# Kernel optimization log

Hardware: AMD Instinct MI355X
Metric: run time of the kernel (lower is better)

## Reference

```python
import jax, jax.numpy as jnp
import numpy as np

H = 16   # num_heads
A = 64   # attn_size
D = 1024 # dims
NEG = -1000000000.0


def setup_inputs() -> dict:
    key = jax.random.key(0)
    k1, k2, k3, k4 = jax.random.split(key, 4)
    B, S = 2, 2048
    qs = jax.random.normal(k1, (B, S, D), dtype=jnp.float32)
    mask = jax.random.randint(k2, (B, S), 0, 2, dtype=jnp.int32)
    Wqkv = jax.random.normal(k3, (D, 3 * H * A), dtype=jnp.float32) * (1.0 / np.sqrt(D))
    Wout = jax.random.normal(k4, (H * A, D), dtype=jnp.float32) * (1.0 / np.sqrt(H * A))
    bout = jnp.zeros((D,), dtype=jnp.float32)
    return {"qs": qs, "mask": mask, "Wqkv": Wqkv, "Wout": Wout, "bout": bout}


def reference(qs, mask, Wqkv, Wout, bout):
    B, S, _ = qs.shape
    qkv = qs @ Wqkv                              # [B,S,3*H*A]
    qkv = qkv.reshape(B, S, 3 * H, A)            # split axis=2 in thirds (TF layout)
    q = jnp.transpose(qkv[:, :, 0:H, :], (0, 2, 1, 3))        # [B,H,S,A]
    k = jnp.transpose(qkv[:, :, H:2 * H, :], (0, 2, 1, 3))    # [B,H,S,A]
    v = jnp.transpose(qkv[:, :, 2 * H:3 * H, :], (0, 2, 1, 3))# [B,H,S,A]
    scores = jnp.einsum('bhqa,bhka->bhqk', q, k) / jnp.sqrt(jnp.float32(A))
    m = mask[:, None, None, :]                   # [B,1,1,S] broadcast over heads, queries
    scores = jnp.where(m == 0, NEG, scores)
    probs = jax.nn.softmax(scores, axis=-1)      # dropout_prob=0 / inference -> identity
    ctx = jnp.einsum('bhqk,bhka->bhqa', probs, v)  # [B,H,S,A]
    ctx = jnp.transpose(ctx, (0, 2, 1, 3)).reshape(B, S, H * A)
    return ctx @ Wout + bout
```

## Files before the change

kernel.cpp:

```cpp
#include <hip/hip_runtime.h>
#include <stdint.h>


typedef unsigned short u16;
typedef uint32_t u32;
typedef u16   u16x4  __attribute__((ext_vector_type(4)));
typedef u16   u16x8  __attribute__((ext_vector_type(8)));
typedef __bf16 bf16x8 __attribute__((ext_vector_type(8)));
typedef float f32x4  __attribute__((ext_vector_type(4)));

#define DEV __device__ __forceinline__

DEV u16 cvt_bf(float f) {
    return __builtin_bit_cast(u16, (__bf16)f);
}

DEV void async16(const void* g, void* l) {
    __builtin_amdgcn_global_load_lds(
        reinterpret_cast<const uint32_t __attribute__((address_space(1)))*>(
            reinterpret_cast<uintptr_t>(g)),
        reinterpret_cast<uint32_t __attribute__((address_space(3)))*>(
            reinterpret_cast<uintptr_t>(l)),
        16, 0, 0);
}

DEV f32x4 mfma16(bf16x8 a, bf16x8 b, f32x4 c) {
    return __builtin_amdgcn_mfma_f32_16x16x32_bf16(a, b, c, 0, 0, 0);
}


__global__ void k_prep(const float* __restrict__ qs, u16* __restrict__ qs_bf,
                       const int* __restrict__ m, float* __restrict__ bias,
                       const float* __restrict__ Wqkv, u16* __restrict__ WqkvT,
                       const float* __restrict__ Wout, u16* __restrict__ WoutT) {
    __shared__ float t[32][33];
    int bid = blockIdx.x;
    if (bid < 4096) {
        int i = (bid * 256 + threadIdx.x) * 4;
        float4 v = *reinterpret_cast<const float4*>(qs + i);
        u16x4 o = { cvt_bf(v.x), cvt_bf(v.y), cvt_bf(v.z), cvt_bf(v.w) };
        *reinterpret_cast<u16x4*>(qs_bf + i) = o;
        return;
    }
    if (bid < 4112) {
        int i = (bid - 4096) * 256 + threadIdx.x;
        bias[i] = m[i] ? 0.0f : -1.0e9f;
        return;
    }
    const float* src; u16* dst; int R, C, bx, by;
    if (bid < 7184) { int q = bid - 4112; src = Wqkv; dst = WqkvT; R = 1024; C = 3072; bx = q % 96; by = q / 96; }
    else            { int q = bid - 7184; src = Wout; dst = WoutT; R = 1024; C = 1024; bx = q % 32; by = q / 32; }
    int c0 = bx * 32, r0 = by * 32;
    int tx = threadIdx.x & 31, ty = threadIdx.x >> 5;
#pragma unroll
    for (int i = 0; i < 4; ++i)
        t[ty + 8 * i][tx] = src[(size_t)(r0 + ty + 8 * i) * C + c0 + tx];
    __syncthreads();
#pragma unroll
    for (int i = 0; i < 4; ++i)
        dst[(size_t)(c0 + ty + 8 * i) * R + r0 + tx] = cvt_bf(t[tx][ty + 8 * i]);
}


template <int BM, int BN, bool OUT_BF16, bool HAS_BIAS>
__global__ __launch_bounds__(256, 3) void k_gemm(
    const u16* __restrict__ A, const u16* __restrict__ Bt,
    void* __restrict__ Cv, const float* __restrict__ bias,
    int M, int N, int K)
{
    constexpr int MT = BM / 32, NT = BN / 32;
    __shared__ __attribute__((aligned(16))) u16 As[2][BM * 32];
    __shared__ __attribute__((aligned(16))) u16 Bs[2][BN * 32];

    const int tid = threadIdx.x, wave = tid >> 6, lane = tid & 63;
    const int lh = lane & 15, lg = lane >> 4;
    const int nbn = N / BN;

    const int nwg = gridDim.x;
    const int q8 = nwg >> 3, r8 = nwg & 7;
    const int xcd = blockIdx.x & 7, li = blockIdx.x >> 3;
    const int wg = (xcd < r8 ? xcd * (q8 + 1) : r8 * (q8 + 1) + (xcd - r8) * q8) + li;

    const int m0 = (wg / nbn) * BM, n0 = (wg % nbn) * BN;
    const int wm = wave >> 1, wn = wave & 1;
    const int nk = K >> 5;

    auto stage = [&](int buf, int kt) {
#pragma unroll
        for (int i = 0; i < BM / 64; ++i) {
            int c = i * 256 + tid;
            int row = c >> 2, cc = c & 3;
            int sc = cc ^ (row & 3);
            async16(A + (size_t)(m0 + row) * K + kt * 32 + sc * 8, &As[buf][c * 8]);
        }
#pragma unroll
        for (int i = 0; i < BN / 64; ++i) {
            int c = i * 256 + tid;
            int row = c >> 2, cc = c & 3;
            int sc = cc ^ (row & 3);
            async16(Bt + (size_t)(n0 + row) * K + kt * 32 + sc * 8, &Bs[buf][c * 8]);
        }
    };

    f32x4 acc[MT][NT] = {};
    stage(0, 0);
    __syncthreads();
    int buf = 0;
    for (int kt = 0; kt < nk; ++kt) {
        if (kt + 1 < nk) stage(buf ^ 1, kt + 1);
        bf16x8 af[MT], bf_[NT];
#pragma unroll
        for (int mt = 0; mt < MT; ++mt) {
            int row = wm * (BM / 2) + mt * 16 + lh;
            int off = row * 32 + ((lg ^ (row & 3)) * 8);
            af[mt] = __builtin_bit_cast(bf16x8,
                     *reinterpret_cast<const u16x8*>(&As[buf][off]));
        }
#pragma unroll
        for (int nt = 0; nt < NT; ++nt) {
            int row = wn * (BN / 2) + nt * 16 + lh;
            int off = row * 32 + ((lg ^ (row & 3)) * 8);
            bf_[nt] = __builtin_bit_cast(bf16x8,
                      *reinterpret_cast<const u16x8*>(&Bs[buf][off]));
        }
        __builtin_amdgcn_s_setprio(1);
#pragma unroll
        for (int mt = 0; mt < MT; ++mt)
#pragma unroll
            for (int nt = 0; nt < NT; ++nt)
                acc[mt][nt] = mfma16(af[mt], bf_[nt], acc[mt][nt]);
        __builtin_amdgcn_s_setprio(0);
        __syncthreads();
        buf ^= 1;
    }

#pragma unroll
    for (int mt = 0; mt < MT; ++mt)
#pragma unroll
        for (int nt = 0; nt < NT; ++nt) {
            int col = n0 + wn * (BN / 2) + nt * 16 + lh;
#pragma unroll
            for (int r = 0; r < 4; ++r) {
                int row = m0 + wm * (BM / 2) + mt * 16 + 4 * lg + r;
                float v = acc[mt][nt][r];
                if (HAS_BIAS) v += bias[col];
                if (OUT_BF16) ((u16*)Cv)[(size_t)row * N + col] = cvt_bf(v);
                else          ((float*)Cv)[(size_t)row * N + col] = v;
            }
        }
}


__global__ __launch_bounds__(512, 4) void k_attn(
    const u16* __restrict__ qkv, const float* __restrict__ biasg, u16* __restrict__ ctx)
{
    __shared__ __attribute__((aligned(16))) u16 Ks[2][64 * 64];
    __shared__ __attribute__((aligned(16))) u16 Vt[2][64 * 72];
    __shared__ __attribute__((aligned(16))) u16 Ps[8 * 16 * 72];

    const int tid = threadIdx.x, wave = tid >> 6, lane = tid & 63;
    const int lh = lane & 15, lg = lane >> 4;

    const int wg = (blockIdx.x & 7) * 64 + (blockIdx.x >> 3);
    const int qt = wg & 15, bh = wg >> 4;
    const int b = bh >> 4, h = bh & 15;

    const u16* qbase = qkv + ((size_t)b * 2048 * 48 + h) * 64;
    const u16* kbase = qkv + ((size_t)b * 2048 * 48 + 16 + h) * 64;
    const u16* vbase = qkv + ((size_t)b * 2048 * 48 + 32 + h) * 64;
    const float* brow = biasg + b * 2048;

    const int srow = wave * 8 + (lane >> 3);
    const int scc  = lane & 7;
    const int ksrc = scc ^ (srow & 7);
    const int vswz = srow ^ (scc << 3);

    bf16x8 qf[2];
    {
        int row = qt * 128 + wave * 16 + lh;
        qf[0] = __builtin_bit_cast(bf16x8,
            *reinterpret_cast<const u16x8*>(qbase + (size_t)row * 3072 + lg * 8));
        qf[1] = __builtin_bit_cast(bf16x8,
            *reinterpret_cast<const u16x8*>(qbase + (size_t)row * 3072 + 32 + lg * 8));
    }

    f32x4 oa[4] = {};
    float lst[4] = {0.0f, 0.0f, 0.0f, 0.0f};

    u16* Pw = &Ps[wave * 16 * 72];

    {
        async16(kbase + (size_t)srow * 3072 + ksrc * 8, &Ks[0][wave * 512]);
        u16x8 v = *reinterpret_cast<const u16x8*>(vbase + (size_t)srow * 3072 + scc * 8);
#pragma unroll
        for (int j = 0; j < 8; ++j) Vt[0][(scc * 8 + j) * 72 + vswz] = v[j];
    }

    for (int kt = 0; kt < 32; ++kt) {
        __syncthreads();
        const int buf = kt & 1;
        if (kt + 1 < 32) {
            async16(kbase + (size_t)((kt + 1) * 64 + srow) * 3072 + ksrc * 8, &Ks[buf ^ 1][wave * 512]);
            u16x8 v = *reinterpret_cast<const u16x8*>(
                vbase + (size_t)((kt + 1) * 64 + srow) * 3072 + scc * 8);
#pragma unroll
            for (int j = 0; j < 8; ++j) Vt[buf ^ 1][(scc * 8 + j) * 72 + vswz] = v[j];
        }

        float biasv[4];
#pragma unroll
        for (int nt = 0; nt < 4; ++nt) biasv[nt] = brow[kt * 64 + nt * 16 + lh];

        f32x4 sa[4] = {};
        __builtin_amdgcn_s_setprio(1);
#pragma unroll
        for (int ks = 0; ks < 2; ++ks) {
            bf16x8 kb[4];
#pragma unroll
            for (int nt = 0; nt < 4; ++nt) {
                int row = nt * 16 + lh;
                int off = row * 64 + (((ks * 4 + lg) ^ (row & 7)) << 3);
                kb[nt] = __builtin_bit_cast(bf16x8,
                         *reinterpret_cast<const u16x8*>(&Ks[buf][off]));
            }
#pragma unroll
            for (int nt = 0; nt < 4; ++nt)
                sa[nt] = mfma16(qf[ks], kb[nt], sa[nt]);
        }
        __builtin_amdgcn_s_setprio(0);

#pragma unroll
        for (int nt = 0; nt < 4; ++nt)
#pragma unroll
            for (int r = 0; r < 4; ++r) {
                float e = __expf(fmaf(sa[nt][r], 0.125f, biasv[nt]));
                lst[r] += e;
                Pw[(4 * lg + r) * 72 + nt * 16 + lh] = cvt_bf(e);
            }

        __builtin_amdgcn_s_setprio(1);
#pragma unroll
        for (int ks = 0; ks < 2; ++ks) {
            bf16x8 pa = __builtin_bit_cast(bf16x8,
                        *reinterpret_cast<const u16x8*>(Pw + lh * 72 + ks * 32 + lg * 8));
            bf16x8 vb[4];
#pragma unroll
            for (int nt = 0; nt < 4; ++nt) {
                int col = nt * 16 + lh;
                int g = (col >> 3) & 7;
                int off = col * 72 + (((ks * 4 + lg) ^ g) << 3);
                vb[nt] = __builtin_bit_cast(bf16x8,
                         *reinterpret_cast<const u16x8*>(&Vt[buf][off]));
            }
#pragma unroll
            for (int nt = 0; nt < 4; ++nt)
                oa[nt] = mfma16(pa, vb[nt], oa[nt]);
        }
        __builtin_amdgcn_s_setprio(0);
    }

#pragma unroll
    for (int r = 0; r < 4; ++r) {
        float s = lst[r];
#pragma unroll
        for (int o = 1; o < 16; o <<= 1) s += __shfl_xor(s, o);
        lst[r] = 1.0f / s;
    }

#pragma unroll
    for (int nt = 0; nt < 4; ++nt)
#pragma unroll
        for (int r = 0; r < 4; ++r) {
            int row = qt * 128 + wave * 16 + 4 * lg + r;
            ctx[(size_t)(b * 2048 + row) * 1024 + h * 64 + nt * 16 + lh] = cvt_bf(oa[nt][r] * lst[r]);
        }
}


extern "C" void kernel_launch(void* const* d_in, const int* in_sizes, int n_in,
                              void* d_out, int out_size, void* d_ws, size_t ws_size,
                              hipStream_t stream)
{
    const float* qs   = (const float*)d_in[0];
    const int*   mask = (const int*)d_in[1];
    const float* Wqkv = (const float*)d_in[2];
    const float* Wout = (const float*)d_in[3];
    const float* bout = (const float*)d_in[4];
    float* out = (float*)d_out;

    char* ws = (char*)d_ws;
    u16*   qs_bf = (u16*)(ws);
    u16*   WqkvT = (u16*)(ws + 8388608);
    u16*   WoutT = (u16*)(ws + 14680064);
    u16*   qkvb  = (u16*)(ws + 16777216);
    u16*   ctxb  = (u16*)(ws + 41943040);
    float* biasb = (float*)(ws + 50331648);

    k_prep<<<8208, 256, 0, stream>>>(qs, qs_bf, mask, biasb, Wqkv, WqkvT, Wout, WoutT);

    k_gemm<128, 128, true, false><<<768, 256, 0, stream>>>(qs_bf, WqkvT, qkvb, nullptr, 4096, 3072, 1024);
    k_attn<<<512, 512, 0, stream>>>(qkvb, biasb, ctxb);
    k_gemm<128, 64, false, true><<<512, 256, 0, stream>>>(ctxb, WoutT, out, bout, 4096, 1024, 1024);
}
```

Baseline: 193.5 us.

## Give each attention wave two query tiles and halve the workgroup size

The attention kernel now runs 4 waves per workgroup instead of 8, and each wave handles 32 query rows (two 16-row MFMA tiles). The K and V fragments read from LDS are then reused across both query tiles, which halves LDS reads per MFMA. The K/V tile loads are split across the fewer threads. In exchange each wave holds more accumulator registers, and the launch bound drops to 3 workgroups per CU, so there are fewer waves available to hide latency.

Measured after the change: 194.8 us. Within noise of the previous version (+0.7%).

```diff
diff --git a/kernel.cpp b/kernel.cpp
--- a/kernel.cpp
+++ b/kernel.cpp
@@ -151,12 +151,12 @@
 }
 
 
-__global__ __launch_bounds__(512, 4) void k_attn(
+__global__ __launch_bounds__(256, 3) void k_attn(
     const u16* __restrict__ qkv, const float* __restrict__ biasg, u16* __restrict__ ctx)
 {
     __shared__ __attribute__((aligned(16))) u16 Ks[2][64 * 64];
     __shared__ __attribute__((aligned(16))) u16 Vt[2][64 * 72];
-    __shared__ __attribute__((aligned(16))) u16 Ps[8 * 16 * 72];
+    __shared__ __attribute__((aligned(16))) u16 Ps[4 * 32 * 72];
 
     const int tid = threadIdx.x, wave = tid >> 6, lane = tid & 63;
     const int lh = lane & 15, lg = lane >> 4;
@@ -170,48 +170,59 @@
     const u16* vbase = qkv + ((size_t)b * 2048 * 48 + 32 + h) * 64;
     const float* brow = biasg + b * 2048;
 
-    const int srow = wave * 8 + (lane >> 3);
-    const int scc  = lane & 7;
-    const int ksrc = scc ^ (srow & 7);
-    const int vswz = srow ^ (scc << 3);
-
-    bf16x8 qf[2];
-    {
-        int row = qt * 128 + wave * 16 + lh;
-        qf[0] = __builtin_bit_cast(bf16x8,
+    int srow_[2], scc_[2];
+#pragma unroll
+    for (int i = 0; i < 2; ++i) {
+        int c = (wave * 2 + i) * 64 + lane;
+        srow_[i] = c >> 3; scc_[i] = c & 7;
+    }
+
+    bf16x8 qf[2][2];
+#pragma unroll
+    for (int mt = 0; mt < 2; ++mt) {
+        int row = qt * 128 + wave * 32 + mt * 16 + lh;
+        qf[mt][0] = __builtin_bit_cast(bf16x8,
             *reinterpret_cast<const u16x8*>(qbase + (size_t)row * 3072 + lg * 8));
-        qf[1] = __builtin_bit_cast(bf16x8,
+        qf[mt][1] = __builtin_bit_cast(bf16x8,
             *reinterpret_cast<const u16x8*>(qbase + (size_t)row * 3072 + 32 + lg * 8));
     }
 
-    f32x4 oa[4] = {};
-    float lst[4] = {0.0f, 0.0f, 0.0f, 0.0f};
-
-    u16* Pw = &Ps[wave * 16 * 72];
-
-    {
-        async16(kbase + (size_t)srow * 3072 + ksrc * 8, &Ks[0][wave * 512]);
+    f32x4 oa[2][4] = {};
+    float lst[2][4] = {};
+
+    u16* Pw = &Ps[wave * 32 * 72];
+
+#pragma unroll
+    for (int i = 0; i < 2; ++i) {
+        int srow = srow_[i], scc = scc_[i];
+        async16(kbase + (size_t)srow * 3072 + (scc ^ (srow & 7)) * 8, &Ks[0][(wave * 2 + i) * 512]);
         u16x8 v = *reinterpret_cast<const u16x8*>(vbase + (size_t)srow * 3072 + scc * 8);
 #pragma unroll
-        for (int j = 0; j < 8; ++j) Vt[0][(scc * 8 + j) * 72 + vswz] = v[j];
+        for (int j = 0; j < 8; ++j) Vt[0][(scc * 8 + j) * 72 + (srow ^ (scc << 3))] = v[j];
     }
 
     for (int kt = 0; kt < 32; ++kt) {
         __syncthreads();
         const int buf = kt & 1;
         if (kt + 1 < 32) {
-            async16(kbase + (size_t)((kt + 1) * 64 + srow) * 3072 + ksrc * 8, &Ks[buf ^ 1][wave * 512]);
-            u16x8 v = *reinterpret_cast<const u16x8*>(
-                vbase + (size_t)((kt + 1) * 64 + srow) * 3072 + scc * 8);
-#pragma unroll
-            for (int j = 0; j < 8; ++j) Vt[buf ^ 1][(scc * 8 + j) * 72 + vswz] = v[j];
+#pragma unroll
+            for (int i = 0; i < 2; ++i) {
+                int srow = srow_[i], scc = scc_[i];
+                async16(kbase + (size_t)((kt + 1) * 64 + srow) * 3072 + (scc ^ (srow & 7)) * 8,
+                        &Ks[buf ^ 1][(wave * 2 + i) * 512]);
+                u16x8 v = *reinterpret_cast<const u16x8*>(
+                    vbase + (size_t)((kt + 1) * 64 + srow) * 3072 + scc * 8);
+#pragma unroll
+                for (int j = 0; j < 8; ++j)
+                    Vt[buf ^ 1][(scc * 8 + j) * 72 + (srow ^ (scc << 3))] = v[j];
+            }
         }
 
         float biasv[4];
 #pragma unroll
         for (int nt = 0; nt < 4; ++nt) biasv[nt] = brow[kt * 64 + nt * 16 + lh];
 
-        f32x4 sa[4] = {};
+        f32x4 sa[2][4] = {};
         __builtin_amdgcn_s_setprio(1);
 #pragma unroll
         for (int ks = 0; ks < 2; ++ks) {
@@ -224,56 +235,68 @@
                          *reinterpret_cast<const u16x8*>(&Ks[buf][off]));
             }
 #pragma unroll
+            for (int mt = 0; mt < 2; ++mt)
+#pragma unroll
+                for (int nt = 0; nt < 4; ++nt)
+                    sa[mt][nt] = mfma16(qf[mt][ks], kb[nt], sa[mt][nt]);
+        }
+        __builtin_amdgcn_s_setprio(0);
+
+#pragma unroll
+        for (int mt = 0; mt < 2; ++mt)
+#pragma unroll
             for (int nt = 0; nt < 4; ++nt)
-                sa[nt] = mfma16(qf[ks], kb[nt], sa[nt]);
-        }
-        __builtin_amdgcn_s_setprio(0);
-
-#pragma unroll
-        for (int nt = 0; nt < 4; ++nt)
-#pragma unroll
-            for (int r = 0; r < 4; ++r) {
-                float e = __expf(fmaf(sa[nt][r], 0.125f, biasv[nt]));
-                lst[r] += e;
-                Pw[(4 * lg + r) * 72 + nt * 16 + lh] = cvt_bf(e);
-            }
+#pragma unroll
+                for (int r = 0; r < 4; ++r) {
+                    float e = __expf(fmaf(sa[mt][nt][r], 0.125f, biasv[nt]));
+                    lst[mt][r] += e;
+                    Pw[(mt * 16 + 4 * lg + r) * 72 + nt * 16 + lh] = cvt_bf(e);
+                }
 
         __builtin_amdgcn_s_setprio(1);
 #pragma unroll
         for (int ks = 0; ks < 2; ++ks) {
-            bf16x8 pa = __builtin_bit_cast(bf16x8,
-                        *reinterpret_cast<const u16x8*>(Pw + lh * 72 + ks * 32 + lg * 8));
-            bf16x8 vb[4];
+            bf16x8 pa[2], vb[4];
+#pragma unroll
+            for (int mt = 0; mt < 2; ++mt)
+                pa[mt] = __builtin_bit_cast(bf16x8,
+                         *reinterpret_cast<const u16x8*>(Pw + (mt * 16 + lh) * 72 + ks * 32 + lg * 8));
 #pragma unroll
             for (int nt = 0; nt < 4; ++nt) {
                 int col = nt * 16 + lh;
-                int g = (col >> 3) & 7;
-                int off = col * 72 + (((ks * 4 + lg) ^ g) << 3);
+                int off = col * 72 + (((ks * 4 + lg) ^ (col >> 3)) << 3);
                 vb[nt] = __builtin_bit_cast(bf16x8,
                          *reinterpret_cast<const u16x8*>(&Vt[buf][off]));
             }
 #pragma unroll
-            for (int nt = 0; nt < 4; ++nt)
-                oa[nt] = mfma16(pa, vb[nt], oa[nt]);
+            for (int mt = 0; mt < 2; ++mt)
+#pragma unroll
+                for (int nt = 0; nt < 4; ++nt)
+                    oa[mt][nt] = mfma16(pa[mt], vb[nt], oa[mt][nt]);
         }
         __builtin_amdgcn_s_setprio(0);
     }
 
 #pragma unroll
-    for (int r = 0; r < 4; ++r) {
-        float s = lst[r];
-#pragma unroll
-        for (int o = 1; o < 16; o <<= 1) s += __shfl_xor(s, o);
-        lst[r] = 1.0f / s;
-    }
-
-#pragma unroll
-    for (int nt = 0; nt < 4; ++nt)
+    for (int mt = 0; mt < 2; ++mt)
 #pragma unroll
         for (int r = 0; r < 4; ++r) {
-            int row = qt * 128 + wave * 16 + 4 * lg + r;
-            ctx[(size_t)(b * 2048 + row) * 1024 + h * 64 + nt * 16 + lh] = cvt_bf(oa[nt][r] * lst[r]);
-        }
+            float s = lst[mt][r];
+#pragma unroll
+            for (int o = 1; o < 16; o <<= 1) s += __shfl_xor(s, o);
+            lst[mt][r] = 1.0f / s;
+        }
+
+#pragma unroll
+    for (int mt = 0; mt < 2; ++mt)
+#pragma unroll
+        for (int nt = 0; nt < 4; ++nt)
+#pragma unroll
+            for (int r = 0; r < 4; ++r) {
+                int row = qt * 128 + wave * 32 + mt * 16 + 4 * lg + r;
+                ctx[(size_t)(b * 2048 + row) * 1024 + h * 64 + nt * 16 + lh] =
+                    cvt_bf(oa[mt][nt][r] * lst[mt][r]);
+            }
 }
 
 
@@ -299,6 +322,6 @@
     k_prep<<<8208, 256, 0, stream>>>(qs, qs_bf, mask, biasb, Wqkv, WqkvT, Wout, WoutT);
 
     k_gemm<128, 128, true, false><<<768, 256, 0, stream>>>(qs_bf, WqkvT, qkvb, nullptr, 4096, 3072, 1024);
-    k_attn<<<512, 512, 0, stream>>>(qkvb, biasb, ctxb);
+    k_attn<<<512, 256, 0, stream>>>(qkvb, biasb, ctxb);
     k_gemm<128, 64, false, true><<<512, 256, 0, stream>>>(ctxb, WoutT, out, bout, 4096, 1024, 1024);
 }
```
